# Performance work log

Measured on AMD Instinct MI355X. Metric: run time of the kernel, lower is better.

Reference implementation:

```python
import jax, jax.numpy as jnp
import numpy as np

N_LAYERS = 2
N_QUBITS = 8
N_MEASURE = 5
DIM = 2 ** N_QUBITS  # 256


def _ry(state, half_theta, wire):
    # Apply RY(theta) = [[cos(t/2), -sin(t/2)], [sin(t/2), cos(t/2)]] on `wire`.
    # Statevector is real (all gates real, initial state real).
    B = state.shape[0]
    st = state.reshape(B, 2 ** wire, 2, 2 ** (N_QUBITS - wire - 1))
    c = jnp.cos(half_theta)[:, None, None]
    s = jnp.sin(half_theta)[:, None, None]
    a0, a1 = st[:, :, 0], st[:, :, 1]
    st = jnp.stack([c * a0 - s * a1, s * a0 + c * a1], axis=2)
    return st.reshape(B, DIM)


def _cnot(state, ctrl):
    # CNOT on wires [ctrl, ctrl+1]: flip target amplitudes where control=1.
    B = state.shape[0]
    st = state.reshape(B, 2 ** ctrl, 2, 2, 2 ** (N_QUBITS - ctrl - 2))
    st = jnp.stack([st[:, :, 0], st[:, :, 1, ::-1]], axis=2)
    return st.reshape(B, DIM)


def setup_inputs() -> dict:
    key = jax.random.key(0)
    k1, k2, k3 = jax.random.split(key, 3)
    B, F = 131072, 16
    inputs = jax.random.normal(k1, (B, F), dtype=jnp.float32)
    weights = jax.random.normal(k2, (N_LAYERS, N_QUBITS), dtype=jnp.float32)
    scalings = jax.random.normal(k3, (N_LAYERS, N_QUBITS), dtype=jnp.float32)
    return {"inputs": inputs, "weights": weights, "scalings": scalings}


def reference(inputs, weights, scalings):
    B, F = inputs.shape
    # |0...0> initial state
    state = jnp.zeros((B, DIM), dtype=inputs.dtype).at[:, 0].set(1.0)
    for layer in range(N_LAYERS):
        start = (layer * N_QUBITS) % F
        for i in range(N_QUBITS):
            fi = (start + i) % F
            theta = weights[layer, i] + scalings[layer, i] * inputs[:, fi]
            state = _ry(state, 0.5 * theta, i)
        for i in range(N_QUBITS - 1):
            state = _cnot(state, i)
    # probs over wires 0..N_MEASURE-1 (marginalize trailing wires)
    probs = (state * state).reshape(B, 2 ** N_MEASURE, 2 ** (N_QUBITS - N_MEASURE)).sum(-1)
    return probs
```

## Files before the change

kernel.cpp:

```cpp
#include <hip/hip_runtime.h>


constexpr int F = 16;

struct Sym { float P, Q, R; };
struct Ent { float up, uq, ur, vp, vq, vr, t, tr2; };

__device__ __forceinline__ Ent mk_ent(float c1, float s1, float c2, float s2) {
    const float u = c2 * c2, v = s2 * s2, t = c2 * s2;
    const float p = c1 * c1, q = s1 * s1, r = c1 * s1;
    Ent e;
    e.up = u * p; e.uq = u * q; e.ur = u * r;
    e.vp = v * p; e.vq = v * q; e.vr = v * r;
    e.t  = t;     e.tr2 = 2.0f * t * r;
    return e;
}

template <int Z>
__device__ __forceinline__ Sym apply_z(const Ent& e, const Sym& s) {
    if (Z == 0) {
        return Sym{ fmaf(e.up, s.P, fmaf(-e.tr2, s.Q, e.vq * s.R)),
                    fmaf(e.ur, s.P, fmaf(-e.t,   s.Q, e.vr * s.R)),
                    fmaf(e.uq, s.P, fmaf(-e.tr2, s.Q, e.vp * s.R)) };
    } else {
        return Sym{ fmaf(e.vp, s.P, fmaf( e.tr2, s.Q, e.uq * s.R)),
                    fmaf(e.vr, s.P, fmaf( e.t,   s.Q, e.ur * s.R)),
                    fmaf(e.vq, s.P, fmaf( e.tr2, s.Q, e.up * s.R)) };
    }
}

__global__ __launch_bounds__(256) void qnn_mps_kernel(
    const float* __restrict__ inputs,
    const float* __restrict__ weights,
    const float* __restrict__ scalings,
    float* __restrict__ out, int B)
{
    const int b = blockIdx.x * 256 + threadIdx.x;
    if (b >= B) return;

    const float4* in4 = reinterpret_cast<const float4*>(inputs) + (size_t)b * 4;
    const float4 xa = in4[0], xb = in4[1], xc = in4[2], xd = in4[3];
    const float x[16] = { xa.x, xa.y, xa.z, xa.w,  xb.x, xb.y, xb.z, xb.w,
                          xc.x, xc.y, xc.z, xc.w,  xd.x, xd.y, xd.z, xd.w };

    float c1[5], s1[5], c2[5], s2[5];
    #pragma unroll
    for (int w = 0; w < 5; ++w) {
        const float t1 = weights[w]     + scalings[w]     * x[w];
        const float t2 = weights[8 + w] + scalings[8 + w] * x[8 + w];
        __sincosf(0.5f * t1, &s1[w], &c1[w]);
        __sincosf(0.5f * t2, &s2[w], &c2[w]);
    }
    const float th5 = weights[5] + scalings[5] * x[5];
    const float s5  = __sinf(th5);

    const Sym r5{ 1.0f, s5, 1.0f };

    const Ent e4 = mk_ent(c1[4], s1[4], c2[4], s2[4]);
    Sym r4[2];
    r4[0] = apply_z<0>(e4, r5);
    r4[1] = apply_z<1>(e4, r5);

    const Ent e3 = mk_ent(c1[3], s1[3], c2[3], s2[3]);
    Sym r3[4];
    r3[0] = apply_z<0>(e3, r4[0]);  r3[1] = apply_z<0>(e3, r4[1]);
    r3[2] = apply_z<1>(e3, r4[0]);  r3[3] = apply_z<1>(e3, r4[1]);

    const Ent e2 = mk_ent(c1[2], s1[2], c2[2], s2[2]);
    Sym r2[8];
    #pragma unroll
    for (int j = 0; j < 4; ++j) {
        r2[j]     = apply_z<0>(e2, r3[j]);
        r2[4 + j] = apply_z<1>(e2, r3[j]);
    }

    const Ent e1 = mk_ent(c1[1], s1[1], c2[1], s2[1]);
    const Ent e0 = mk_ent(c1[0], s1[0], c2[0], s2[0]);

    float pr[32];
    #pragma unroll
    for (int j = 0; j < 8; ++j) {
        #pragma unroll
        for (int z1 = 0; z1 < 2; ++z1) {
            const Sym v = (z1 == 0) ? apply_z<0>(e1, r2[j]) : apply_z<1>(e1, r2[j]);
            #pragma unroll
            for (int z0 = 0; z0 < 2; ++z0) {
                const float p = (z0 == 0)
                    ? fmaf(e0.up, v.P, fmaf(-e0.tr2, v.Q, e0.vq * v.R))
                    : fmaf(e0.vp, v.P, fmaf( e0.tr2, v.Q, e0.uq * v.R));
                const int Z = (z0 << 4) | (z1 << 3) | j;
                int G = Z; G ^= G >> 1; G ^= G >> 2; G ^= G >> 4;
                pr[G & 31] = p;
            }
        }
    }

    float4* o4 = reinterpret_cast<float4*>(out) + (size_t)b * 8;
    #pragma unroll
    for (int i = 0; i < 8; ++i)
        o4[i] = make_float4(pr[4 * i], pr[4 * i + 1], pr[4 * i + 2], pr[4 * i + 3]);
}

extern "C" void kernel_launch(void* const* d_in, const int* in_sizes, int n_in,
                              void* d_out, int out_size, void* d_ws, size_t ws_size,
                              hipStream_t stream) {
    const float* inputs   = (const float*)d_in[0];
    const float* weights  = (const float*)d_in[1];
    const float* scalings = (const float*)d_in[2];
    float* out = (float*)d_out;
    const int B = in_sizes[0] / F;
    const int grid = (B + 255) / 256;
    qnn_mps_kernel<<<grid, 256, 0, stream>>>(inputs, weights, scalings, out, B);
}
```

Before: 70.38 us.

## Split each batch row across four threads, each producing eight output probabilities

Each batch element is now handled by four threads instead of one. Every thread redundantly computes the shared trig and upper contraction levels, then evaluates only its own branch of the last levels and writes two float4s. Output stores become contiguous across neighbouring threads, and per-thread register pressure drops, which should raise occupancy. The cost is duplicated input loads and trig work, repeated four times per row.

After: 68.57 us. -2.6%, faster.

```diff
diff --git a/kernel.cpp b/kernel.cpp
--- a/kernel.cpp
+++ b/kernel.cpp
@@ -5,6 +5,7 @@
 
 struct Sym { float P, Q, R; };
 struct Ent { float up, uq, ur, vp, vq, vr, t, tr2; };
+struct Eff { float A, B, C, D, E, Fc, G, H; };
 
 __device__ __forceinline__ Ent mk_ent(float c1, float s1, float c2, float s2) {
     const float u = c2 * c2, v = s2 * s2, t = c2 * s2;
@@ -29,14 +30,37 @@
     }
 }
 
-__global__ __launch_bounds__(256) void qnn_mps_kernel(
+__device__ __forceinline__ Eff mk_eff(const Ent& e, bool z) {
+    Eff f;
+    f.A = z ? e.vp  :  e.up;   f.B = z ? e.tr2 : -e.tr2;
+    f.C = z ? e.uq  :  e.vq;   f.D = z ? e.vr  :  e.ur;
+    f.E = z ? e.t   : -e.t;    f.Fc= z ? e.ur  :  e.vr;
+    f.G = z ? e.vq  :  e.uq;   f.H = z ? e.up  :  e.vp;
+    return f;
+}
+__device__ __forceinline__ Eff flip_eff(const Eff& e) {
+    return Eff{ e.H, -e.B, e.G, e.Fc, -e.E, e.D, e.C, e.A };
+}
+__device__ __forceinline__ Sym apply_eff(const Eff& e, const Sym& s) {
+    return Sym{ fmaf(e.A, s.P, fmaf(e.B, s.Q, e.C  * s.R)),
+                fmaf(e.D, s.P, fmaf(e.E, s.Q, e.Fc * s.R)),
+                fmaf(e.G, s.P, fmaf(e.B, s.Q, e.H  * s.R)) };
+}
+
+__global__ __launch_bounds__(256) void qnn_mps4_kernel(
     const float* __restrict__ inputs,
     const float* __restrict__ weights,
     const float* __restrict__ scalings,
     float* __restrict__ out, int B)
 {
-    const int b = blockIdx.x * 256 + threadIdx.x;
+    const int g = blockIdx.x * 256 + threadIdx.x;
+    const int b = g >> 2;
+    const int t = g & 3;
     if (b >= B) return;
+
+    const bool z0 = (t >> 1) & 1;
+    const bool z1 = ((t ^ (t >> 1)) & 1);
+    const bool tb = (t & 1);
 
     const float4* in4 = reinterpret_cast<const float4*>(inputs) + (size_t)b * 4;
     const float4 xa = in4[0], xb = in4[1], xc = in4[2], xd = in4[3];
@@ -67,38 +91,32 @@
     r3[2] = apply_z<1>(e3, r4[0]);  r3[3] = apply_z<1>(e3, r4[1]);
 
     const Ent e2 = mk_ent(c1[2], s1[2], c2[2], s2[2]);
-    Sym r2[8];
+    const Eff e2a = mk_eff(e2, tb);
+    const Eff e2b = flip_eff(e2a);
+    Sym r2p[8];
     #pragma unroll
     for (int j = 0; j < 4; ++j) {
-        r2[j]     = apply_z<0>(e2, r3[j]);
-        r2[4 + j] = apply_z<1>(e2, r3[j]);
+        r2p[j]     = apply_eff(e2a, r3[j]);
+        r2p[4 + j] = apply_eff(e2b, r3[j]);
     }
 
-    const Ent e1 = mk_ent(c1[1], s1[1], c2[1], s2[1]);
-    const Ent e0 = mk_ent(c1[0], s1[0], c2[0], s2[0]);
+    const Eff e1e = mk_eff(mk_ent(c1[1], s1[1], c2[1], s2[1]), z1);
+    const Ent e0  = mk_ent(c1[0], s1[0], c2[0], s2[0]);
+    const float A0 = z0 ? e0.vp  :  e0.up;
+    const float B0 = z0 ? e0.tr2 : -e0.tr2;
+    const float C0 = z0 ? e0.uq  :  e0.vq;
 
-    float pr[32];
+    float pr[8];
     #pragma unroll
-    for (int j = 0; j < 8; ++j) {
-        #pragma unroll
-        for (int z1 = 0; z1 < 2; ++z1) {
-            const Sym v = (z1 == 0) ? apply_z<0>(e1, r2[j]) : apply_z<1>(e1, r2[j]);
-            #pragma unroll
-            for (int z0 = 0; z0 < 2; ++z0) {
-                const float p = (z0 == 0)
-                    ? fmaf(e0.up, v.P, fmaf(-e0.tr2, v.Q, e0.vq * v.R))
-                    : fmaf(e0.vp, v.P, fmaf( e0.tr2, v.Q, e0.uq * v.R));
-                const int Z = (z0 << 4) | (z1 << 3) | j;
-                int G = Z; G ^= G >> 1; G ^= G >> 2; G ^= G >> 4;
-                pr[G & 31] = p;
-            }
-        }
+    for (int u = 0; u < 8; ++u) {
+        constexpr int gray[8] = {0, 1, 3, 2, 6, 7, 5, 4};
+        const Sym v = apply_eff(e1e, r2p[gray[u]]);
+        pr[u] = fmaf(A0, v.P, fmaf(B0, v.Q, C0 * v.R));
     }
 
-    float4* o4 = reinterpret_cast<float4*>(out) + (size_t)b * 8;
-    #pragma unroll
-    for (int i = 0; i < 8; ++i)
-        o4[i] = make_float4(pr[4 * i], pr[4 * i + 1], pr[4 * i + 2], pr[4 * i + 3]);
+    float4* o4 = reinterpret_cast<float4*>(out) + (size_t)b * 8 + (size_t)t * 2;
+    o4[0] = make_float4(pr[0], pr[1], pr[2], pr[3]);
+    o4[1] = make_float4(pr[4], pr[5], pr[6], pr[7]);
 }
 
 extern "C" void kernel_launch(void* const* d_in, const int* in_sizes, int n_in,
@@ -109,6 +127,7 @@
     const float* scalings = (const float*)d_in[2];
     float* out = (float*)d_out;
     const int B = in_sizes[0] / F;
-    const int grid = (B + 255) / 256;
-    qnn_mps_kernel<<<grid, 256, 0, stream>>>(inputs, weights, scalings, out, B);
+    const int total = B * 4;
+    const int grid = (total + 255) / 256;
+    qnn_mps4_kernel<<<grid, 256, 0, stream>>>(inputs, weights, scalings, out, B);
 }
```
